# Optimization experiments

Measured on AMD Instinct MI355X. Metric: run time of the kernel, lower is better.

The kernel has to match this reference:

```python
import jax, jax.numpy as jnp
import numpy as np

H = 768  # HIDDEN_SIZE


def setup_inputs() -> dict:
    key = jax.random.key(0)
    ks = jax.random.split(key, 6)
    B, T = 32, 1024
    W_SCALE = 0.05  # keep gate pre-activations out of deep saturation
    return {
        "input": jax.random.normal(ks[0], (B, T, H), dtype=jnp.float32),
        "hidden_state": jax.random.normal(ks[1], (1, B, H), dtype=jnp.float32),
        "W_ih": jax.random.normal(ks[2], (3 * H, H), dtype=jnp.float32) * W_SCALE,
        "W_hh": jax.random.normal(ks[3], (3 * H, H), dtype=jnp.float32) * W_SCALE,
        "b_ih": jax.random.normal(ks[4], (3 * H,), dtype=jnp.float32) * W_SCALE,
        "b_hh": jax.random.normal(ks[5], (3 * H,), dtype=jnp.float32) * W_SCALE,
    }


def reference(input, hidden_state, W_ih, W_hh, b_ih, b_hh):
    # PyTorch GRU gate order in the stacked weights is (r, z, n).
    # The module fills bias_ih[H:2H] and bias_hh[H:2H] with -inf, so
    # z_t = sigmoid(-inf) = 0 exactly and h_t = n_t. We therefore skip the
    # structurally-dead z rows entirely (same math, fewer FLOPs):
    #   r_t = sigmoid(W_ir x_t + b_ir + W_hr h_{t-1} + b_hr)
    #   h_t = tanh(W_in x_t + b_in + r_t * (W_hn h_{t-1} + b_hn))
    W_ir, W_in = W_ih[:H], W_ih[2 * H:]          # [H, H] each
    W_hr, W_hn = W_hh[:H], W_hh[2 * H:]
    b_ir, b_in = b_ih[:H], b_ih[2 * H:]
    b_hr, b_hn = b_hh[:H], b_hh[2 * H:]

    # Input projections for all timesteps at once: [B, T, H] each.
    gi_r = jnp.einsum("bth,gh->btg", input, W_ir) + b_ir
    gi_n = jnp.einsum("bth,gh->btg", input, W_in) + b_in

    h0 = hidden_state[0]  # [B, H]

    def step(h, gi_t):
        gi_r_t, gi_n_t = gi_t  # [B, H] each
        r = jax.nn.sigmoid(gi_r_t + h @ W_hr.T + b_hr)
        h_new = jnp.tanh(gi_n_t + r * (h @ W_hn.T + b_hn))
        return h_new, h_new

    # scan over time: move T to leading axis.
    xs = (jnp.swapaxes(gi_r, 0, 1), jnp.swapaxes(gi_n, 0, 1))  # [T, B, H]
    _, hs = jax.lax.scan(step, h0, xs)
    return jnp.swapaxes(hs, 0, 1)  # [B, T, H]
```

## Files before the change

### kernel.cpp

```cpp
#include <hip/hip_runtime.h>
#include <hip/hip_bf16.h>

#define Hd 768
#define Bd 32
#define Td 1024
#define Md (Bd*Td)

#define NPAIR 16
#define SPW   16
#define GPW   48
#define THRS  384
#define RINGD 4
#define SENT_U 0x7FC00000u
#define RVALS (2*Hd)

typedef unsigned int u32x4 __attribute__((ext_vector_type(4)));
typedef float f32x2 __attribute__((ext_vector_type(2)));

static __device__ __forceinline__ f32x2 splat2(float v) { f32x2 r; r.x = v; r.y = v; return r; }

__global__ __launch_bounds__(256) void k_init(const float* __restrict__ hid,
                                              unsigned* __restrict__ ring) {
    int i = blockIdx.x * 256 + threadIdx.x;
    const int p   = i / (RINGD * RVALS);
    const int rem = i % (RINGD * RVALS);
    const int r   = rem / RVALS;
    const int q   = rem % RVALS;
    const int bb  = q / Hd;
    const int k   = q % Hd;
    unsigned v = SENT_U;
    if (r == 0) v = ((const unsigned*)hid)[(p * 2 + bb) * Hd + k];
    ring[i] = v;
}

__global__ __launch_bounds__(256, 2) void k_gemm(const float* __restrict__ A,
                                                 const float* __restrict__ Wih,
                                                 const float* __restrict__ bih,
                                                 float* __restrict__ giR,
                                                 float* __restrict__ giN) {
    __shared__ float As[16][68];
    __shared__ float Brs[16][68];
    __shared__ float Bns[16][68];
    const int tid = threadIdx.x;
    const int mb = blockIdx.x & 511;
    const int nb = blockIdx.x >> 9;
    const int lm = tid >> 2;
    const int lk = (tid & 3) << 2;
    const int tx = tid & 15;
    const int ty = tid >> 4;

    const float* pA = A   + (size_t)(mb * 64 + lm) * Hd + lk;
    const float* pR = Wih + (size_t)(nb * 64 + lm) * Hd + lk;
    const float* pN = Wih + (size_t)(2 * Hd + nb * 64 + lm) * Hd + lk;

    float accR[4][4] = {{0.f}};
    float accN[4][4] = {{0.f}};

    for (int kt = 0; kt < Hd; kt += 16) {
        float4 va = *(const float4*)(pA + kt);
        float4 vr = *(const float4*)(pR + kt);
        float4 vn = *(const float4*)(pN + kt);
        __syncthreads();
        As[lk+0][lm]=va.x; As[lk+1][lm]=va.y; As[lk+2][lm]=va.z; As[lk+3][lm]=va.w;
        Brs[lk+0][lm]=vr.x; Brs[lk+1][lm]=vr.y; Brs[lk+2][lm]=vr.z; Brs[lk+3][lm]=vr.w;
        Bns[lk+0][lm]=vn.x; Bns[lk+1][lm]=vn.y; Bns[lk+2][lm]=vn.z; Bns[lk+3][lm]=vn.w;
        __syncthreads();
        #pragma unroll
        for (int k = 0; k < 16; ++k) {
            float4 a4 = *(const float4*)&As[k][ty << 2];
            float4 r4 = *(const float4*)&Brs[k][tx << 2];
            float4 n4 = *(const float4*)&Bns[k][tx << 2];
            float av[4] = {a4.x, a4.y, a4.z, a4.w};
            float rv[4] = {r4.x, r4.y, r4.z, r4.w};
            float nv[4] = {n4.x, n4.y, n4.z, n4.w};
            #pragma unroll
            for (int i = 0; i < 4; ++i)
                #pragma unroll
                for (int j = 0; j < 4; ++j) {
                    accR[i][j] += av[i] * rv[j];
                    accN[i][j] += av[i] * nv[j];
                }
        }
    }

    const int m0 = mb * 64 + (ty << 2);
    const int g0 = nb * 64 + (tx << 2);
    float4 bR = *(const float4*)(bih + g0);
    float4 bN = *(const float4*)(bih + 2 * Hd + g0);
    #pragma unroll
    for (int i = 0; i < 4; ++i) {
        float4 oR = { accR[i][0]+bR.x, accR[i][1]+bR.y, accR[i][2]+bR.z, accR[i][3]+bR.w };
        float4 oN = { accN[i][0]+bN.x, accN[i][1]+bN.y, accN[i][2]+bN.z, accN[i][3]+bN.w };
        *(float4*)(giR + (size_t)(m0 + i) * Hd + g0) = oR;
        *(float4*)(giN + (size_t)(m0 + i) * Hd + g0) = oN;
    }
}

#define ALLJ(M, q) M(q,0) M(q,1) M(q,2) M(q,3) M(q,4) M(q,5) M(q,6) M(q,7) M(q,8) M(q,9) M(q,10) M(q,11)

#define WDECL(q,j) f32x2 w##q##_##j##_0, w##q##_##j##_1, w##q##_##j##_2, w##q##_##j##_3;

#define WLOAD(q,j) { \
    const float4 _a = *(const float4*)(pwr##q + (j << 6)); \
    const float4 _b = *(const float4*)(pwn##q + (j << 6)); \
    w##q##_##j##_0.x=_a.x; w##q##_##j##_0.y=_b.x; \
    w##q##_##j##_1.x=_a.y; w##q##_##j##_1.y=_b.y; \
    w##q##_##j##_2.x=_a.z; w##q##_##j##_2.y=_b.z; \
    w##q##_##j##_3.x=_a.w; w##q##_##j##_3.y=_b.w; }

#define WPIN(q,j) asm volatile("" : "+v"(w##q##_##j##_0), "+v"(w##q##_##j##_1), \
                                    "+v"(w##q##_##j##_2), "+v"(w##q##_##j##_3));

#define WFMA(q,j,A) \
    A = __builtin_elementwise_fma(splat2(h4.x), w##q##_##j##_0, A); \
    A = __builtin_elementwise_fma(splat2(h4.y), w##q##_##j##_1, A); \
    A = __builtin_elementwise_fma(splat2(h4.z), w##q##_##j##_2, A); \
    A = __builtin_elementwise_fma(splat2(h4.w), w##q##_##j##_3, A);

#define DOJ(A0,A1,bb,j) { \
    const float4 h4 = *(const float4*)&hsl[bb * Hd + kofs + (j << 6)]; \
    WFMA(0,j,A0) WFMA(1,j,A1) }

#define ALLJ2(M,A0,A1,bb) M(A0,A1,bb,0) M(A0,A1,bb,1) M(A0,A1,bb,2) M(A0,A1,bb,3) \
    M(A0,A1,bb,4) M(A0,A1,bb,5) M(A0,A1,bb,6) M(A0,A1,bb,7) \
    M(A0,A1,bb,8) M(A0,A1,bb,9) M(A0,A1,bb,10) M(A0,A1,bb,11)

#define BFLY(A) \
    A.x += __shfl_xor(A.x, 8); A.y += __shfl_xor(A.y, 8); \
    A.x += __shfl_xor(A.x, 4); A.y += __shfl_xor(A.y, 4); \
    A.x += __shfl_xor(A.x, 2); A.y += __shfl_xor(A.y, 2); \
    A.x += __shfl_xor(A.x, 1); A.y += __shfl_xor(A.y, 1);

__global__ __launch_bounds__(THRS)
__attribute__((amdgpu_waves_per_eu(2, 2)))
void k_scan(const float* __restrict__ Whh,
            const float* __restrict__ bhh,
            const float* __restrict__ giR,
            float* __restrict__ out,
            unsigned* __restrict__ ring) {
    __shared__ float hs[2 * RVALS];
    const int tid = threadIdx.x;
    const int gl  = tid >> 4;
    const int ks  = tid & 15;
    const int p   = blockIdx.x >> 4;
    const int s   = blockIdx.x & 15;
    const int b0  = p * 2;
    const int kofs = ks << 2;
    unsigned* ringp = ring + (size_t)p * RINGD * RVALS;

    const float* pwr0 = Whh + (size_t)(s * GPW + gl) * Hd + kofs;
    const float* pwr1 = Whh + (size_t)(s * GPW + 24 + gl) * Hd + kofs;
    const float* pwn0 = pwr0 + (size_t)2 * Hd * Hd;
    const float* pwn1 = pwr1 + (size_t)2 * Hd * Hd;

    ALLJ(WDECL, 0) ALLJ(WDECL, 1)
    ALLJ(WLOAD, 0) ALLJ(WLOAD, 1)
    ALLJ(WPIN, 0)  ALLJ(WPIN, 1)

    const int osub = ks & 1, obb = ks >> 1;
    const int og   = s * GPW + osub * 24 + gl;
    float obr = 0.f, obn = 0.f, gRv = 0.f, gNv = 0.f;
    if (ks < 4) {
        obr = bhh[og];
        obn = bhh[2 * Hd + og];
        const size_t mi = ((size_t)(b0 + obb) * Td) * Hd + og;
        gRv = giR[mi];
        gNv = out[mi];
    }

    for (int t = 0; t < Td; ++t) {
        const unsigned* myp = ringp + (t & 3) * RVALS + (tid << 2);
        float* hsl = hs + (t & 1) * RVALS;
        u32x4 w;
        asm volatile("global_load_dwordx4 %0, %1, off sc0 sc1\n\ts_waitcnt vmcnt(0)"
                     : "=v"(w) : "v"(myp) : "memory");
        while (w.x == SENT_U || w.y == SENT_U || w.z == SENT_U || w.w == SENT_U) {
            __builtin_amdgcn_s_sleep(1);
            asm volatile("global_load_dwordx4 %0, %1, off sc0 sc1\n\ts_waitcnt vmcnt(0)"
                         : "=v"(w) : "v"(myp) : "memory");
        }
        *(u32x4*)((unsigned*)hsl + (tid << 2)) = w;

        float gR2 = 0.f, gN2 = 0.f;
        if (ks < 4) {
            const unsigned* rp = ringp + ((t + 2) & 3) * RVALS + obb * Hd + og;
            unsigned sv = SENT_U;
            asm volatile("global_store_dword %0, %1, off sc0 sc1"
                         :: "v"(rp), "v"(sv) : "memory");
            if (t + 1 < Td) {
                const size_t mi = ((size_t)(b0 + obb) * Td + (t + 1)) * Hd + og;
                gR2 = giR[mi];
                gN2 = out[mi];
            }
        }

        __syncthreads();

        f32x2 a00 = splat2(0.f), a01 = splat2(0.f), a10 = splat2(0.f), a11 = splat2(0.f);
        ALLJ2(DOJ, a00, a10, 0)
        ALLJ2(DOJ, a01, a11, 1)
        BFLY(a00) BFLY(a01) BFLY(a10) BFLY(a11)

        float hnew = 0.f;
        if (ks < 4) {
            f32x2 mine = osub ? (obb ? a11 : a10) : (obb ? a01 : a00);
            const float r = 1.f / (1.f + __expf(-(gRv + mine.x + obr)));
            hnew = tanhf(gNv + r * (mine.y + obn));
            gRv = gR2; gNv = gN2;
        }

        asm volatile("s_waitcnt vmcnt(0)" ::: "memory");

        if (ks < 4) {
            const unsigned* dp = ringp + ((t + 1) & 3) * RVALS + obb * Hd + og;
            const unsigned hbits = __float_as_uint(hnew);
            asm volatile("global_store_dword %0, %1, off sc0 sc1"
                         :: "v"(dp), "v"(hbits) : "memory");
            out[((size_t)(b0 + obb) * Td + t) * Hd + og] = hnew;
        }
    }
}

extern "C" void kernel_launch(void* const* d_in, const int* in_sizes, int n_in,
                              void* d_out, int out_size, void* d_ws, size_t ws_size,
                              hipStream_t stream) {
    const float* input  = (const float*)d_in[0];
    const float* hidden = (const float*)d_in[1];
    const float* Wih    = (const float*)d_in[2];
    const float* Whh    = (const float*)d_in[3];
    const float* bih    = (const float*)d_in[4];
    const float* bhh    = (const float*)d_in[5];
    float* out = (float*)d_out;

    float*    giR  = (float*)d_ws;
    unsigned* ring = (unsigned*)(giR + (size_t)Md * Hd);

    k_init<<<(NPAIR * RINGD * RVALS) / 256, 256, 0, stream>>>(hidden, ring);
    k_gemm<<<512 * 12, 256, 0, stream>>>(input, Wih, bih, giR, out);
    k_scan<<<NPAIR * SPW, THRS, 0, stream>>>(Whh, bhh, giR, out, ring);
}
```

Measured before the change: 4.879 ms.

## Stream bf16-packed recurrent weights from cache each step instead of register-pinning

A new pre-pass packs the W_hr and W_hn rows into interleaved bf16 pairs. The scan kernel no longer holds fp32 weights in registers; it reloads the packed weights from global memory every timestep and overlaps those loads with the FMA loop using staged waitcnts. The sentinel reset now uses one vectorized store per thread after the barrier. This frees many VGPRs but adds per-step L2 traffic and bf16 rounding error on the recurrent weights, which can accumulate over 1024 steps.

```diff
diff --git a/kernel.cpp b/kernel.cpp
--- a/kernel.cpp
+++ b/kernel.cpp
@@ -31,6 +31,20 @@
     unsigned v = SENT_U;
     if (r == 0) v = ((const unsigned*)hid)[(p * 2 + bb) * Hd + k];
     ring[i] = v;
+}
+
+static __device__ __forceinline__ unsigned bf16rne(float f) {
+    unsigned x = __float_as_uint(f);
+    return (x + 0x7FFFu + ((x >> 16) & 1u)) >> 16;
+}
+__global__ __launch_bounds__(256) void k_pack(const float* __restrict__ Whh,
+                                              unsigned* __restrict__ wpk) {
+    int i = blockIdx.x * 256 + threadIdx.x;
+    if (i >= Hd * Hd) return;
+    const int g = i / Hd, k = i % Hd;
+    const unsigned lo = bf16rne(Whh[(size_t)g * Hd + k]);
+    const unsigned hi = bf16rne(Whh[(size_t)(2 * Hd + g) * Hd + k]);
+    wpk[i] = lo | (hi << 16);
 }
 
 __global__ __launch_bounds__(256, 2) void k_gemm(const float* __restrict__ A,
@@ -98,32 +112,21 @@
 
 #define ALLJ(M, q) M(q,0) M(q,1) M(q,2) M(q,3) M(q,4) M(q,5) M(q,6) M(q,7) M(q,8) M(q,9) M(q,10) M(q,11)
 
-#define WDECL(q,j) f32x2 w##q##_##j##_0, w##q##_##j##_1, w##q##_##j##_2, w##q##_##j##_3;
-
-#define WLOAD(q,j) { \
-    const float4 _a = *(const float4*)(pwr##q + (j << 6)); \
-    const float4 _b = *(const float4*)(pwn##q + (j << 6)); \
-    w##q##_##j##_0.x=_a.x; w##q##_##j##_0.y=_b.x; \
-    w##q##_##j##_1.x=_a.y; w##q##_##j##_1.y=_b.y; \
-    w##q##_##j##_2.x=_a.z; w##q##_##j##_2.y=_b.z; \
-    w##q##_##j##_3.x=_a.w; w##q##_##j##_3.y=_b.w; }
-
-#define WPIN(q,j) asm volatile("" : "+v"(w##q##_##j##_0), "+v"(w##q##_##j##_1), \
-                                    "+v"(w##q##_##j##_2), "+v"(w##q##_##j##_3));
-
-#define WFMA(q,j,A) \
-    A = __builtin_elementwise_fma(splat2(h4.x), w##q##_##j##_0, A); \
-    A = __builtin_elementwise_fma(splat2(h4.y), w##q##_##j##_1, A); \
-    A = __builtin_elementwise_fma(splat2(h4.z), w##q##_##j##_2, A); \
-    A = __builtin_elementwise_fma(splat2(h4.w), w##q##_##j##_3, A);
-
-#define DOJ(A0,A1,bb,j) { \
-    const float4 h4 = *(const float4*)&hsl[bb * Hd + kofs + (j << 6)]; \
-    WFMA(0,j,A0) WFMA(1,j,A1) }
-
-#define ALLJ2(M,A0,A1,bb) M(A0,A1,bb,0) M(A0,A1,bb,1) M(A0,A1,bb,2) M(A0,A1,bb,3) \
-    M(A0,A1,bb,4) M(A0,A1,bb,5) M(A0,A1,bb,6) M(A0,A1,bb,7) \
-    M(A0,A1,bb,8) M(A0,A1,bb,9) M(A0,A1,bb,10) M(A0,A1,bb,11)
+#define WDECL(q,j) u32x4 w##q##_##j;
+#define WISSUE(q,j) asm volatile("global_load_dwordx4 %0, %1, off" \
+    : "=v"(w##q##_##j) : "v"(pw##q + (j << 6)) : "memory");
+
+#define CVT1(q,j,C,HC0,HC1) { \
+    const unsigned _p = w##q##_##j.C; \
+    f32x2 _wv; _wv.x = __uint_as_float(_p << 16); _wv.y = __uint_as_float(_p & 0xFFFF0000u); \
+    a##q##_0 = __builtin_elementwise_fma(splat2(HC0), _wv, a##q##_0); \
+    a##q##_1 = __builtin_elementwise_fma(splat2(HC1), _wv, a##q##_1); }
+
+#define DOJ(q,j) { \
+    const float4 _h0 = *(const float4*)&hsl[kofs + (j << 6)]; \
+    const float4 _h1 = *(const float4*)&hsl[Hd + kofs + (j << 6)]; \
+    CVT1(q,j,x,_h0.x,_h1.x) CVT1(q,j,y,_h0.y,_h1.y) \
+    CVT1(q,j,z,_h0.z,_h1.z) CVT1(q,j,w,_h0.w,_h1.w) }
 
 #define BFLY(A) \
     A.x += __shfl_xor(A.x, 8); A.y += __shfl_xor(A.y, 8); \
@@ -133,7 +136,7 @@
 
 __global__ __launch_bounds__(THRS)
 __attribute__((amdgpu_waves_per_eu(2, 2)))
-void k_scan(const float* __restrict__ Whh,
+void k_scan(const unsigned* __restrict__ wpk,
             const float* __restrict__ bhh,
             const float* __restrict__ giR,
             float* __restrict__ out,
@@ -148,14 +151,8 @@
     const int kofs = ks << 2;
     unsigned* ringp = ring + (size_t)p * RINGD * RVALS;
 
-    const float* pwr0 = Whh + (size_t)(s * GPW + gl) * Hd + kofs;
-    const float* pwr1 = Whh + (size_t)(s * GPW + 24 + gl) * Hd + kofs;
-    const float* pwn0 = pwr0 + (size_t)2 * Hd * Hd;
-    const float* pwn1 = pwr1 + (size_t)2 * Hd * Hd;
-
-    ALLJ(WDECL, 0) ALLJ(WDECL, 1)
-    ALLJ(WLOAD, 0) ALLJ(WLOAD, 1)
-    ALLJ(WPIN, 0)  ALLJ(WPIN, 1)
+    const unsigned* pw0 = wpk + (size_t)(s * GPW + gl) * Hd + kofs;
+    const unsigned* pw1 = wpk + (size_t)(s * GPW + 24 + gl) * Hd + kofs;
 
     const int osub = ks & 1, obb = ks >> 1;
     const int og   = s * GPW + osub * 24 + gl;
@@ -181,37 +178,55 @@
         }
         *(u32x4*)((unsigned*)hsl + (tid << 2)) = w;
 
+        __syncthreads();
+
+        {
+            const unsigned* rp = ringp + ((t + 2) & 3) * RVALS + (tid << 2);
+            u32x4 sv = { SENT_U, SENT_U, SENT_U, SENT_U };
+            asm volatile("global_store_dwordx4 %0, %1, off sc0 sc1"
+                         :: "v"(rp), "v"(sv) : "memory");
+        }
+
+        WDECL(0,0) WDECL(0,1) WDECL(0,2) WDECL(0,3) WDECL(0,4) WDECL(0,5)
+        WDECL(0,6) WDECL(0,7) WDECL(0,8) WDECL(0,9) WDECL(0,10) WDECL(0,11)
+        WDECL(1,0) WDECL(1,1) WDECL(1,2) WDECL(1,3) WDECL(1,4) WDECL(1,5)
+        WDECL(1,6) WDECL(1,7) WDECL(1,8) WDECL(1,9) WDECL(1,10) WDECL(1,11)
+        ALLJ(WISSUE, 0)
+        ALLJ(WISSUE, 1)
+
         float gR2 = 0.f, gN2 = 0.f;
+        {
+            const int tn = (t + 1 < Td) ? t + 1 : t;
+            if (ks < 4) {
+                const size_t mi = ((size_t)(b0 + obb) * Td + tn) * Hd + og;
+                asm volatile("global_load_dword %0, %1, off"
+                             : "=v"(gR2) : "v"(giR + mi) : "memory");
+                asm volatile("global_load_dword %0, %1, off"
+                             : "=v"(gN2) : "v"(out + mi) : "memory");
+            }
+        }
+
+        asm volatile("s_waitcnt vmcnt(14)" ::: "memory");
+        __builtin_amdgcn_sched_barrier(0);
+
+        f32x2 a0_0 = splat2(0.f), a0_1 = splat2(0.f);
+        f32x2 a1_0 = splat2(0.f), a1_1 = splat2(0.f);
+        ALLJ(DOJ, 0)
+
+        asm volatile("s_waitcnt vmcnt(2)" ::: "memory");
+        __builtin_amdgcn_sched_barrier(0);
+        ALLJ(DOJ, 1)
+
+        BFLY(a0_0) BFLY(a0_1) BFLY(a1_0) BFLY(a1_1)
+
+        asm volatile("s_waitcnt vmcnt(0)" ::: "memory");
+        __builtin_amdgcn_sched_barrier(0);
+
         if (ks < 4) {
-            const unsigned* rp = ringp + ((t + 2) & 3) * RVALS + obb * Hd + og;
-            unsigned sv = SENT_U;
-            asm volatile("global_store_dword %0, %1, off sc0 sc1"
-                         :: "v"(rp), "v"(sv) : "memory");
-            if (t + 1 < Td) {
-                const size_t mi = ((size_t)(b0 + obb) * Td + (t + 1)) * Hd + og;
-                gR2 = giR[mi];
-                gN2 = out[mi];
-            }
-        }
-
-        __syncthreads();
-
-        f32x2 a00 = splat2(0.f), a01 = splat2(0.f), a10 = splat2(0.f), a11 = splat2(0.f);
-        ALLJ2(DOJ, a00, a10, 0)
-        ALLJ2(DOJ, a01, a11, 1)
-        BFLY(a00) BFLY(a01) BFLY(a10) BFLY(a11)
-
-        float hnew = 0.f;
-        if (ks < 4) {
-            f32x2 mine = osub ? (obb ? a11 : a10) : (obb ? a01 : a00);
+            f32x2 mine = osub ? (obb ? a1_1 : a1_0) : (obb ? a0_1 : a0_0);
             const float r = 1.f / (1.f + __expf(-(gRv + mine.x + obr)));
-            hnew = tanhf(gNv + r * (mine.y + obn));
+            const float hnew = tanhf(gNv + r * (mine.y + obn));
             gRv = gR2; gNv = gN2;
-        }
-
-        asm volatile("s_waitcnt vmcnt(0)" ::: "memory");
-
-        if (ks < 4) {
             const unsigned* dp = ringp + ((t + 1) & 3) * RVALS + obb * Hd + og;
             const unsigned hbits = __float_as_uint(hnew);
             asm volatile("global_store_dword %0, %1, off sc0 sc1"
@@ -234,8 +249,10 @@
 
     float*    giR  = (float*)d_ws;
     unsigned* ring = (unsigned*)(giR + (size_t)Md * Hd);
+    unsigned* wpk  = ring + (size_t)NPAIR * RINGD * RVALS;
 
     k_init<<<(NPAIR * RINGD * RVALS) / 256, 256, 0, stream>>>(hidden, ring);
+    k_pack<<<(Hd * Hd + 255) / 256, 256, 0, stream>>>(Whh, wpk);
     k_gemm<<<512 * 12, 256, 0, stream>>>(input, Wih, bih, giR, out);
-    k_scan<<<NPAIR * SPW, THRS, 0, stream>>>(Whh, bhh, giR, out, ring);
-}
+    k_scan<<<NPAIR * SPW, THRS, 0, stream>>>(wpk, bhh, giR, out, ring);
+}
```

After: 6.629 ms. 1.36x slower.
